# Optimization experiments

Measured on AMD Instinct MI355X. Metric: run time of the kernel, lower is better.

## Reference

```python
import jax, jax.numpy as jnp
import numpy as np

EPS = 1e-3    # Keras BatchNormalization default epsilon
ALPHA = 0.3   # Keras LeakyReLU default negative slope


def _bn(x, axes):
    # BatchNormalization(center=False, scale=False) in training mode: batch stats
    m = jnp.mean(x, axis=axes, keepdims=True)
    v = jnp.var(x, axis=axes, keepdims=True)
    return (x - m) * jax.lax.rsqrt(v + EPS)


def _leaky(x):
    return jnp.where(x > 0, x, ALPHA * x)


def setup_inputs() -> dict:
    key = jax.random.key(0)
    ks = jax.random.split(key, 8)
    B, A, D, Hid, H, hd = 8192, 16, 256, 512, 8, 64
    s = 0.02
    return {
        "state": jax.random.normal(ks[0], (B, A, D), jnp.float32),
        "agent_index": 3,
        "Ws": jax.random.normal(ks[1], (D, Hid), jnp.float32) * s,
        "bs": jnp.zeros((Hid,), jnp.float32),
        "Wc": jax.random.normal(ks[2], (D, Hid), jnp.float32) * s,
        "bc": jnp.zeros((Hid,), jnp.float32),
        "Wk": jax.random.normal(ks[3], (H, Hid, hd), jnp.float32) * s,
        "Wq": jax.random.normal(ks[4], (H, Hid, hd), jnp.float32) * s,
        "Wv": jax.random.normal(ks[5], (H, Hid, hd), jnp.float32) * s,
    }


def reference(state, agent_index, Ws, bs, Wc, bc, Wk, Wq, Wv):
    B = state.shape[0]
    H, _, hd = Wk.shape
    ai = int(agent_index)

    # current agent encoder: BN over batch, Dense, LeakyReLU -> [B, Hid]
    cur = state[:, ai, :]
    s_enc = _leaky(_bn(cur, (0,)) @ Ws + bs)

    # other agents encoder: BN over (batch, agent), Dense, LeakyReLU -> [B, A-1, Hid]
    others = jnp.concatenate([state[:, :ai, :], state[:, ai + 1:, :]], axis=1)
    sa_enc = _leaky(_bn(others, (0, 1)) @ Wc + bc)

    # batched per-head projections (replaces the python loop over heads)
    k = jnp.einsum('ban,hnd->bhad', sa_enc, Wk)           # [B,H,A-1,hd]
    v = _leaky(jnp.einsum('ban,hnd->bhad', sa_enc, Wv))   # [B,H,A-1,hd]
    q = jnp.einsum('bn,hnd->bhd', s_enc, Wq)              # [B,H,hd]

    scores = jnp.einsum('bhd,bhad->bha', q, k) / jnp.sqrt(jnp.float32(hd))
    w = jax.nn.softmax(scores, axis=-1)                   # [B,H,A-1]
    att = jnp.einsum('bha,bhad->bhd', w, v)               # [B,H,hd]

    # concat heads in order -> [B, H*hd]
    return att.reshape(B, H * hd)
```

## Files before the change

kernel.cpp:

```cpp
#include <hip/hip_runtime.h>

typedef __attribute__((ext_vector_type(8))) short short8;
typedef __attribute__((ext_vector_type(8))) unsigned short ushort8;
typedef __attribute__((ext_vector_type(4))) unsigned short bfu4;
typedef __attribute__((ext_vector_type(4))) float f32x4;

__device__ __forceinline__ unsigned short f2bf(float f){
  unsigned int u = __builtin_bit_cast(unsigned int, f);
  u += 0x7fffu + ((u >> 16) & 1u);
  return (unsigned short)(u >> 16);
}
__device__ __forceinline__ float bf2f(unsigned short h){
  unsigned int u = ((unsigned int)h) << 16;
  return __builtin_bit_cast(float, u);
}
__device__ __forceinline__ float leaky(float x){ return x > 0.f ? x : 0.3f * x; }

#define SAS 520

__global__ __launch_bounds__(1024) void ca_stats_partial(const float* __restrict__ state,
    const int* __restrict__ agp, float* __restrict__ part, int B){
  int d = threadIdx.x & 255, sl = threadIdx.x >> 8;
  int ag = agp[0];
  int bPer = (B + 255) >> 8;
  int b0 = blockIdx.x * bPer;
  float sC = 0.f, ssC = 0.f, sO = 0.f, ssO = 0.f;
  for (int b = sl; b < bPer; b += 4){
    int bb = b0 + b;
    if (bb >= B) continue;
    const float* row = state + ((size_t)bb << 12);
    #pragma unroll
    for (int a = 0; a < 16; a++){
      float v = row[a*256 + d];
      bool isC = (a == ag);
      sC  += isC ? v   : 0.f;
      ssC += isC ? v*v : 0.f;
      sO  += isC ? 0.f : v;
      ssO += isC ? 0.f : v*v;
    }
  }
  __shared__ float red[4][4][256];
  red[sl][0][d] = sC; red[sl][1][d] = ssC; red[sl][2][d] = sO; red[sl][3][d] = ssO;
  __syncthreads();
  if (sl == 0){
    float* p = part + (size_t)blockIdx.x * 1024;
    p[d]     = red[0][0][d] + red[1][0][d] + red[2][0][d] + red[3][0][d];
    p[d+256] = red[0][1][d] + red[1][1][d] + red[2][1][d] + red[3][1][d];
    p[d+512] = red[0][2][d] + red[1][2][d] + red[2][2][d] + red[3][2][d];
    p[d+768] = red[0][3][d] + red[1][3][d] + red[2][3][d] + red[3][3][d];
  }
}

__global__ __launch_bounds__(1024) void ca_stats_final(const float* __restrict__ part,
    float* __restrict__ stats, int nblk, int B){
  int d = threadIdx.x & 255, sl = threadIdx.x >> 8;
  float sC = 0.f, ssC = 0.f, sO = 0.f, ssO = 0.f;
  for (int g = sl; g < nblk; g += 4){
    const float* p = part + (size_t)g * 1024;
    sC += p[d]; ssC += p[d+256]; sO += p[d+512]; ssO += p[d+768];
  }
  __shared__ float red[4][4][256];
  red[sl][0][d] = sC; red[sl][1][d] = ssC; red[sl][2][d] = sO; red[sl][3][d] = ssO;
  __syncthreads();
  if (sl == 0){
    sC  = red[0][0][d] + red[1][0][d] + red[2][0][d] + red[3][0][d];
    ssC = red[0][1][d] + red[1][1][d] + red[2][1][d] + red[3][1][d];
    sO  = red[0][2][d] + red[1][2][d] + red[2][2][d] + red[3][2][d];
    ssO = red[0][3][d] + red[1][3][d] + red[2][3][d] + red[3][3][d];
    float nC = (float)B, nO = (float)B * 15.f;
    float mC = sC / nC, vC = ssC / nC - mC * mC;
    float mO = sO / nO, vO = ssO / nO - mO * mO;
    float rC = rsqrtf(vC + 1e-3f), rO = rsqrtf(vO + 1e-3f);
    stats[d] = rC; stats[d+256] = mC * rC; stats[d+512] = rO; stats[d+768] = mO * rO;
  }
}

__global__ __launch_bounds__(256) void ca_prep_sc(const float* __restrict__ Ws,
    const float* __restrict__ bs, const float* __restrict__ Wc, const float* __restrict__ bc,
    const float* __restrict__ stats, unsigned short* __restrict__ WsT,
    unsigned short* __restrict__ WcT, unsigned short* __restrict__ WsF,
    unsigned short* __restrict__ WcF, float* __restrict__ bsp, float* __restrict__ bcp){
  int n = blockIdx.x, d = threadIdx.x;
  float rC = stats[d], mrC = stats[d+256], rO = stats[d+512], mrO = stats[d+768];
  float ws = Ws[(size_t)d*512 + n], wc = Wc[(size_t)d*512 + n];
  unsigned short wsb = f2bf(ws * rC), wcb = f2bf(wc * rO);
  WsT[(size_t)n*256 + d] = wsb;
  WcT[(size_t)n*256 + d] = wcb;
  {
    int h = n >> 6, nt = (n >> 4) & 3, j = n & 15;
    int kk = d >> 5, hi = (d >> 3) & 3, e = d & 7;
    size_t fi = (size_t)((h*8 + kk)*4 + nt)*512 + (hi*16 + j)*8 + e;
    WsF[fi] = wsb;
    WcF[fi] = wcb;
  }
  __shared__ float red[256];
  red[d] = mrC * ws;
  __syncthreads();
  for (int s = 128; s > 0; s >>= 1){ if (d < s) red[d] += red[d+s]; __syncthreads(); }
  if (d == 0) bsp[n] = bs[n] - red[0];
  __syncthreads();
  red[d] = mrO * wc;
  __syncthreads();
  for (int s = 128; s > 0; s >>= 1){ if (d < s) red[d] += red[d+s]; __syncthreads(); }
  if (d == 0) bcp[n] = bc[n] - red[0];
}

__global__ __launch_bounds__(512) void ca_prep_kvq(const float* __restrict__ Wk,
    const float* __restrict__ Wv, const float* __restrict__ Wq,
    unsigned short* __restrict__ WkT, unsigned short* __restrict__ WvT,
    unsigned short* __restrict__ WqT, unsigned short* __restrict__ WkF2,
    unsigned short* __restrict__ WvF, unsigned short* __restrict__ WqF){
  int c = blockIdx.x & 511, m = blockIdx.x >> 9;
  int n = threadIdx.x;
  if (m == 3){
    size_t idx = (size_t)c*512 + n;
    int h = (int)(idx >> 15), nn = (int)((idx >> 6) & 511), dd = (int)(idx & 63);
    int nt = nn >> 4, j = nn & 15, kq = dd >> 5, hi = (dd >> 3) & 3, e = dd & 7;
    WkF2[(size_t)((h*32 + nt)*2 + kq)*512 + (hi*16 + j)*8 + e] = f2bf(Wk[idx]);
    return;
  }
  int h = c >> 6, dd = c & 63;
  const float* W = (m == 0) ? Wk : (m == 1) ? Wv : Wq;
  unsigned short* O = (m == 0) ? WkT : (m == 1) ? WvT : WqT;
  float scale = (m == 2) ? 0.125f : 1.f;
  unsigned short v = f2bf(W[((size_t)h*512 + n)*64 + dd] * scale);
  O[(size_t)c*512 + n] = v;
  if (m != 0){
    int nt = (c >> 4) & 3, j = c & 15;
    int kk = n >> 5, hi = (n >> 3) & 3, e = n & 7;
    size_t fi = (size_t)((h*16 + kk)*4 + nt)*512 + (hi*16 + j)*8 + e;
    if (m == 1) WvF[fi] = v; else WqF[fi] = v;
  }
}

__global__ __launch_bounds__(512) void ca_q_kernel(const float* __restrict__ state,
    const int* __restrict__ agp,
    const unsigned short* __restrict__ WsT, const float* __restrict__ bsp,
    const unsigned short* __restrict__ WqT, unsigned short* __restrict__ Qws){
  __shared__ unsigned short U[32*512];
  __shared__ float bias_s[512];
  unsigned short* Alds = U;
  unsigned short* SE = U;
  int tid = threadIdx.x, lane = tid & 63, w = tid >> 6;
  int j = lane & 15, hi = lane >> 4;
  int b0 = blockIdx.x * 32;
  int ag = agp[0];

  for (int s = tid; s < 32*32; s += 512){
    int row = s >> 5, kg = s & 31;
    const float* p = state + (((size_t)(b0 + row) * 16 + ag) << 8) + kg * 8;
    f32x4 v0 = *(const f32x4*)p, v1 = *(const f32x4*)(p + 4);
    ushort8 hv;
    hv[0]=f2bf(v0[0]); hv[1]=f2bf(v0[1]); hv[2]=f2bf(v0[2]); hv[3]=f2bf(v0[3]);
    hv[4]=f2bf(v1[0]); hv[5]=f2bf(v1[1]); hv[6]=f2bf(v1[2]); hv[7]=f2bf(v1[3]);
    *(ushort8*)&Alds[row*256 + ((kg ^ (row & 7)) << 3)] = hv;
  }
  bias_s[tid & 511] = bsp[tid & 511];
  __syncthreads();

  int cb = w * 64;
  f32x4 zero4 = {0.f, 0.f, 0.f, 0.f};
  f32x4 acc[2][4];
  #pragma unroll
  for (int a1 = 0; a1 < 2; a1++)
    #pragma unroll
    for (int a2 = 0; a2 < 4; a2++) acc[a1][a2] = zero4;

  #pragma unroll
  for (int kk = 0; kk < 8; kk++){
    short8 bfr[4];
    #pragma unroll
    for (int nt = 0; nt < 4; nt++)
      bfr[nt] = *(const short8*)&WsT[(size_t)(cb + nt*16 + j)*256 + kk*32 + hi*8];
    #pragma unroll
    for (int mt = 0; mt < 2; mt++){
      int row = mt*16 + j;
      short8 afr = *(const short8*)&Alds[row*256 + ((((kk << 2) | hi) ^ (row & 7)) << 3)];
      #pragma unroll
      for (int nt = 0; nt < 4; nt++)
        acc[mt][nt] = __builtin_amdgcn_mfma_f32_16x16x32_bf16(afr, bfr[nt], acc[mt][nt], 0, 0, 0);
    }
  }
  __syncthreads();
  #pragma unroll
  for (int mt = 0; mt < 2; mt++)
    #pragma unroll
    for (int nt = 0; nt < 4; nt++)
      #pragma unroll
      for (int i = 0; i < 4; i++){
        int row = mt*16 + hi*4 + i, col = cb + nt*16 + j;
        float x = leaky(acc[mt][nt][i] + bias_s[col]);
        SE[row*512 + ((((col >> 3) ^ (row & 7)) << 3) | (col & 7))] = f2bf(x);
      }
  __syncthreads();

  f32x4 qa[2][4];
  #pragma unroll
  for (int a1 = 0; a1 < 2; a1++)
    #pragma unroll
    for (int a2 = 0; a2 < 4; a2++) qa[a1][a2] = zero4;
  #pragma unroll
  for (int kk = 0; kk < 16; kk++){
    short8 bfr[4];
    #pragma unroll
    for (int nt = 0; nt < 4; nt++)
      bfr[nt] = *(const short8*)&WqT[(size_t)(cb + nt*16 + j)*512 + kk*32 + hi*8];
    #pragma unroll
    for (int mt = 0; mt < 2; mt++){
      int row = mt*16 + j;
      short8 afr = *(const short8*)&SE[row*512 + ((((kk << 2) | hi) ^ (row & 7)) << 3)];
      #pragma unroll
      for (int nt = 0; nt < 4; nt++)
        qa[mt][nt] = __builtin_amdgcn_mfma_f32_16x16x32_bf16(afr, bfr[nt], qa[mt][nt], 0, 0, 0);
    }
  }
  #pragma unroll
  for (int mt = 0; mt < 2; mt++)
    #pragma unroll
    for (int nt = 0; nt < 4; nt++)
      #pragma unroll
      for (int i = 0; i < 4; i++)
        Qws[(size_t)(b0 + mt*16 + hi*4 + i)*512 + cb + nt*16 + j] = f2bf(qa[mt][nt][i]);
}

__global__ __launch_bounds__(512) void ca_q_kernel_qk(const float* __restrict__ state,
    const int* __restrict__ agp,
    const unsigned short* __restrict__ WsF, const float* __restrict__ bsp,
    const unsigned short* __restrict__ WqF, const unsigned short* __restrict__ WkF2,
    unsigned short* __restrict__ QKws){
  __shared__ unsigned short U[16*SAS];
  __shared__ float bias_s[512];
  unsigned short* Alds = U;
  unsigned short* SE = U;
  unsigned short* Qlds = U;
  int tid = threadIdx.x, lane = tid & 63, w = tid >> 6;
  int j = lane & 15, hi = lane >> 4;
  int b0 = blockIdx.x * 16;
  int ag = agp[0];
  f32x4 zero4 = {0.f, 0.f, 0.f, 0.f};

  {
    int row = tid >> 5, kg = tid & 31;
    const float* p = state + (((size_t)(b0 + row) * 16 + ag) << 8) + kg * 8;
    f32x4 v0 = *(const f32x4*)p, v1 = *(const f32x4*)(p + 4);
    ushort8 hv;
    hv[0]=f2bf(v0[0]); hv[1]=f2bf(v0[1]); hv[2]=f2bf(v0[2]); hv[3]=f2bf(v0[3]);
    hv[4]=f2bf(v1[0]); hv[5]=f2bf(v1[1]); hv[6]=f2bf(v1[2]); hv[7]=f2bf(v1[3]);
    *(ushort8*)&Alds[row*256 + ((kg ^ (row & 7)) << 3)] = hv;
  }
  bias_s[tid] = bsp[tid];
  __syncthreads();

  int cb = w * 64;

  f32x4 acc[4];
  #pragma unroll
  for (int a2 = 0; a2 < 4; a2++) acc[a2] = zero4;
  #pragma unroll
  for (int kk = 0; kk < 8; kk++){
    short8 bfr[4];
    #pragma unroll
    for (int nt = 0; nt < 4; nt++)
      bfr[nt] = *(const short8*)&WsF[(size_t)((w*8 + kk)*4 + nt)*512 + lane*8];
    short8 afr = *(const short8*)&Alds[j*256 + ((((kk << 2) | hi) ^ (j & 7)) << 3)];
    #pragma unroll
    for (int nt = 0; nt < 4; nt++)
      acc[nt] = __builtin_amdgcn_mfma_f32_16x16x32_bf16(bfr[nt], afr, acc[nt], 0, 0, 0);
  }
  __syncthreads();
  #pragma unroll
  for (int nt = 0; nt < 4; nt++){
    int nb = cb + nt*16 + hi*4;
    bfu4 pk;
    #pragma unroll
    for (int i = 0; i < 4; i++) pk[i] = f2bf(leaky(acc[nt][i] + bias_s[nb + i]));
    *(bfu4*)&SE[j*SAS + nb] = pk;
  }
  __syncthreads();

  f32x4 qa[4];
  #pragma unroll
  for (int a2 = 0; a2 < 4; a2++) qa[a2] = zero4;
  #pragma unroll
  for (int kk = 0; kk < 16; kk++){
    short8 bfr[4];
    #pragma unroll
    for (int nt = 0; nt < 4; nt++)
      bfr[nt] = *(const short8*)&WqF[(size_t)((w*16 + kk)*4 + nt)*512 + lane*8];
    short8 afr = *(const short8*)&SE[j*SAS + kk*32 + hi*8];
    #pragma unroll
    for (int nt = 0; nt < 4; nt++)
      qa[nt] = __builtin_amdgcn_mfma_f32_16x16x32_bf16(bfr[nt], afr, qa[nt], 0, 0, 0);
  }
  __syncthreads();
  #pragma unroll
  for (int nt = 0; nt < 4; nt++){
    int nb = cb + nt*16 + hi*4;
    bfu4 pk;
    #pragma unroll
    for (int i = 0; i < 4; i++) pk[i] = f2bf(qa[nt][i]);
    *(bfu4*)&Qlds[j*SAS + nb] = pk;
  }
  __syncthreads();

  short8 aq[2];
  #pragma unroll
  for (int kq = 0; kq < 2; kq++)
    aq[kq] = *(const short8*)&Qlds[j*SAS + w*64 + kq*32 + hi*8];
  for (int nt = 0; nt < 32; nt++){
    short8 bf0 = *(const short8*)&WkF2[(size_t)((w*32 + nt)*2 + 0)*512 + lane*8];
    short8 bf1 = *(const short8*)&WkF2[(size_t)((w*32 + nt)*2 + 1)*512 + lane*8];
    f32x4 qt = zero4;
    qt = __builtin_amdgcn_mfma_f32_16x16x32_bf16(bf0, aq[0], qt, 0, 0, 0);
    qt = __builtin_amdgcn_mfma_f32_16x16x32_bf16(bf1, aq[1], qt, 0, 0, 0);
    bfu4 pk;
    pk[0] = f2bf(qt[0]); pk[1] = f2bf(qt[1]); pk[2] = f2bf(qt[2]); pk[3] = f2bf(qt[3]);
    *(bfu4*)&QKws[((size_t)(b0 + j)*8 + w)*512 + nt*16 + hi*4] = pk;
  }
}

__global__ __launch_bounds__(512) void ca_main_kernel_qk(const float* __restrict__ state,
    const int* __restrict__ agp,
    const unsigned short* __restrict__ WcF, const float* __restrict__ bcp,
    const unsigned short* __restrict__ WvF, const unsigned short* __restrict__ QKws,
    float* __restrict__ out){
  __shared__ unsigned short U[128*SAS];
  __shared__ float bias_s[512];
  __shared__ float Wl[8*16*8];
  unsigned short* Alds = U;
  unsigned short* SA = U;
  int tid = threadIdx.x, lane = tid & 63, w = tid >> 6;
  int j = lane & 15, hi = lane >> 4;
  int b0 = blockIdx.x * 8;
  int ag = agp[0];
  f32x4 zero4 = {0.f, 0.f, 0.f, 0.f};
  short8 zero8 = {0,0,0,0,0,0,0,0};

  #pragma unroll
  for (int g = 0; g < 2; g++){
    f32x4 st0[4], st1[4];
    #pragma unroll
    for (int it = 0; it < 4; it++){
      int s = tid + 512*(g*4 + it);
      int row = s >> 5, kg = s & 31;
      int bl = row >> 4, ai = row & 15;
      if (ai < 15){
        int a = ai + (ai >= ag ? 1 : 0);
        const float* p = state + (((size_t)(b0 + bl) * 16 + a) << 8) + kg * 8;
        st0[it] = *(const f32x4*)p;
        st1[it] = *(const f32x4*)(p + 4);
      } else { st0[it] = zero4; st1[it] = zero4; }
    }
    #pragma unroll
    for (int it = 0; it < 4; it++){
      int s = tid + 512*(g*4 + it);
      int row = s >> 5, kg = s & 31;
      ushort8 hv;
      hv[0]=f2bf(st0[it][0]); hv[1]=f2bf(st0[it][1]); hv[2]=f2bf(st0[it][2]); hv[3]=f2bf(st0[it][3]);
      hv[4]=f2bf(st1[it][0]); hv[5]=f2bf(st1[it][1]); hv[6]=f2bf(st1[it][2]); hv[7]=f2bf(st1[it][3]);
      *(ushort8*)&Alds[row*256 + ((kg ^ (row & 7)) << 3)] = hv;
    }
  }
  bias_s[tid] = bcp[tid];
  __syncthreads();

  int cb = w * 64;

  f32x4 acc[8][4];
  #pragma unroll
  for (int a1 = 0; a1 < 8; a1++)
    #pragma unroll
    for (int a2 = 0; a2 < 4; a2++) acc[a1][a2] = zero4;
  {
    short8 bcur[4], bnxt[4];
    #pragma unroll
    for (int nt = 0; nt < 4; nt++)
      bcur[nt] = *(const short8*)&WcF[(size_t)((w*8 + 0)*4 + nt)*512 + lane*8];
    #pragma unroll 1
    for (int kk = 0; kk < 8; kk++){
      if (kk < 7){
        #pragma unroll
        for (int nt = 0; nt < 4; nt++)
          bnxt[nt] = *(const short8*)&WcF[(size_t)((w*8 + kk + 1)*4 + nt)*512 + lane*8];
      }
      #pragma unroll
      for (int mt = 0; mt < 8; mt++){
        int row = mt*16 + j;
        short8 afr = *(const short8*)&Alds[row*256 + ((((kk << 2) | hi) ^ (row & 7)) << 3)];
        #pragma unroll
        for (int nt = 0; nt < 4; nt++)
          acc[mt][nt] = __builtin_amdgcn_mfma_f32_16x16x32_bf16(bcur[nt], afr, acc[mt][nt], 0, 0, 0);
      }
      #pragma unroll
      for (int nt = 0; nt < 4; nt++) bcur[nt] = bnxt[nt];
    }
  }
  __syncthreads();
  #pragma unroll
  for (int mt = 0; mt < 8; mt++)
    #pragma unroll
    for (int nt = 0; nt < 4; nt++){
      int m = mt*16 + j;
      int nb = cb + nt*16 + hi*4;
      bfu4 pk;
      #pragma unroll
      for (int i = 0; i < 4; i++) pk[i] = f2bf(leaky(acc[mt][nt][i] + bias_s[nb + i]));
      *(bfu4*)&SA[m*SAS + nb] = pk;
    }
  __syncthreads();

  f32x4 qs = zero4;
  {
    size_t qbase = ((size_t)(b0 + w)*8 + (j & 7))*512;
    #pragma unroll
    for (int kk = 0; kk < 16; kk++){
      short8 bq = *(const short8*)&QKws[qbase + kk*32 + hi*8];
      if (j >= 8) bq = zero8;
      short8 afr = *(const short8*)&SA[(w*16 + j)*SAS + kk*32 + hi*8];
      qs = __builtin_amdgcn_mfma_f32_16x16x32_bf16(afr, bq, qs, 0, 0, 0);
    }
  }
  {
    float sv0 = qs[0], sv1 = qs[1], sv2 = qs[2], sv3 = qs[3];
    sv3 = (hi == 3) ? -1e30f : sv3;
    float m = fmaxf(fmaxf(sv0, sv1), fmaxf(sv2, sv3));
    m = fmaxf(m, __shfl_xor(m, 16)); m = fmaxf(m, __shfl_xor(m, 32));
    float e0 = __expf(sv0-m), e1 = __expf(sv1-m), e2 = __expf(sv2-m), e3 = __expf(sv3-m);
    float sum = e0 + e1 + e2 + e3;
    sum += __shfl_xor(sum, 16); sum += __shfl_xor(sum, 32);
    float inv = 1.f / sum;
    if (j < 8){
      Wl[w*128 + (hi*4+0)*8 + j] = e0*inv;
      Wl[w*128 + (hi*4+1)*8 + j] = e1*inv;
      Wl[w*128 + (hi*4+2)*8 + j] = e2*inv;
      Wl[w*128 + (hi*4+3)*8 + j] = e3*inv;
    }
  }

  f32x4 va[8][4];
  #pragma unroll
  for (int a1 = 0; a1 < 8; a1++)
    #pragma unroll
    for (int a2 = 0; a2 < 4; a2++) va[a1][a2] = zero4;
  {
    short8 bcur[4], bnxt[4];
    #pragma unroll
    for (int nt = 0; nt < 4; nt++)
      bcur[nt] = *(const short8*)&WvF[(size_t)((w*16 + 0)*4 + nt)*512 + lane*8];
    #pragma unroll 1
    for (int kk = 0; kk < 16; kk++){
      if (kk < 15){
        #pragma unroll
        for (int nt = 0; nt < 4; nt++)
          bnxt[nt] = *(const short8*)&WvF[(size_t)((w*16 + kk + 1)*4 + nt)*512 + lane*8];
      }
      #pragma unroll
      for (int mt = 0; mt < 8; mt++){
        short8 afr = *(const short8*)&SA[(mt*16 + j)*SAS + kk*32 + hi*8];
        #pragma unroll
        for (int nt = 0; nt < 4; nt++)
          va[mt][nt] = __builtin_amdgcn_mfma_f32_16x16x32_bf16(afr, bcur[nt], va[mt][nt], 0, 0, 0);
      }
      #pragma unroll
      for (int nt = 0; nt < 4; nt++) bcur[nt] = bnxt[nt];
    }
  }
  __syncthreads();

  #pragma unroll
  for (int mt = 0; mt < 8; mt++){
    float w0 = Wl[mt*128 + (hi*4+0)*8 + w];
    float w1 = Wl[mt*128 + (hi*4+1)*8 + w];
    float w2 = Wl[mt*128 + (hi*4+2)*8 + w];
    float w3 = Wl[mt*128 + (hi*4+3)*8 + w];
    float ap0 = w0*leaky(va[mt][0][0]) + w1*leaky(va[mt][0][1]) + w2*leaky(va[mt][0][2]) + w3*leaky(va[mt][0][3]);
    float ap1 = w0*leaky(va[mt][1][0]) + w1*leaky(va[mt][1][1]) + w2*leaky(va[mt][1][2]) + w3*leaky(va[mt][1][3]);
    float ap2 = w0*leaky(va[mt][2][0]) + w1*leaky(va[mt][2][1]) + w2*leaky(va[mt][2][2]) + w3*leaky(va[mt][2][3]);
    float ap3 = w0*leaky(va[mt][3][0]) + w1*leaky(va[mt][3][1]) + w2*leaky(va[mt][3][2]) + w3*leaky(va[mt][3][3]);
    ap0 += __shfl_xor(ap0, 16); ap0 += __shfl_xor(ap0, 32);
    ap1 += __shfl_xor(ap1, 16); ap1 += __shfl_xor(ap1, 32);
    ap2 += __shfl_xor(ap2, 16); ap2 += __shfl_xor(ap2, 32);
    ap3 += __shfl_xor(ap3, 16); ap3 += __shfl_xor(ap3, 32);
    float val = (hi == 0) ? ap0 : (hi == 1) ? ap1 : (hi == 2) ? ap2 : ap3;
    out[(size_t)(b0 + mt)*512 + cb + lane] = val;
  }
}

__global__ __launch_bounds__(512) void ca_main_kernel(const float* __restrict__ state,
    const int* __restrict__ agp,
    const unsigned short* __restrict__ WcT, const float* __restrict__ bcp,
    const unsigned short* __restrict__ WkT, const unsigned short* __restrict__ WvT,
    const unsigned short* __restrict__ Qws, float* __restrict__ out){
  __shared__ unsigned short U[128*512];
  __shared__ unsigned short Qs[8*512];
  __shared__ float bias_s[512];
  unsigned short* Alds = U;
  unsigned short* SA = U;
  int tid = threadIdx.x, lane = tid & 63, w = tid >> 6;
  int j = lane & 15, hi = lane >> 4;
  int b0 = blockIdx.x * 8;
  int ag = agp[0];
  f32x4 zero4 = {0.f, 0.f, 0.f, 0.f};

  #pragma unroll
  for (int g = 0; g < 2; g++){
    f32x4 st0[4], st1[4];
    #pragma unroll
    for (int it = 0; it < 4; it++){
      int s = tid + 512*(g*4 + it);
      int row = s >> 5, kg = s & 31;
      int bl = row >> 4, ai = row & 15;
      if (ai < 15){
        int a = ai + (ai >= ag ? 1 : 0);
        const float* p = state + (((size_t)(b0 + bl) * 16 + a) << 8) + kg * 8;
        st0[it] = *(const f32x4*)p;
        st1[it] = *(const f32x4*)(p + 4);
      } else { st0[it] = zero4; st1[it] = zero4; }
    }
    #pragma unroll
    for (int it = 0; it < 4; it++){
      int s = tid + 512*(g*4 + it);
      int row = s >> 5, kg = s & 31;
      ushort8 hv;
      hv[0]=f2bf(st0[it][0]); hv[1]=f2bf(st0[it][1]); hv[2]=f2bf(st0[it][2]); hv[3]=f2bf(st0[it][3]);
      hv[4]=f2bf(st1[it][0]); hv[5]=f2bf(st1[it][1]); hv[6]=f2bf(st1[it][2]); hv[7]=f2bf(st1[it][3]);
      *(ushort8*)&Alds[row*256 + ((kg ^ (row & 7)) << 3)] = hv;
    }
  }
  *(ushort8*)&Qs[tid*8] = *(const ushort8*)&Qws[(size_t)b0*512 + tid*8];
  bias_s[tid] = bcp[tid];
  __syncthreads();

  int cb = w * 64;

  f32x4 acc[8][4];
  #pragma unroll
  for (int a1 = 0; a1 < 8; a1++)
    #pragma unroll
    for (int a2 = 0; a2 < 4; a2++) acc[a1][a2] = zero4;
  {
    short8 bcur[4], bnxt[4];
    #pragma unroll
    for (int nt = 0; nt < 4; nt++)
      bcur[nt] = *(const short8*)&WcT[(size_t)(cb + nt*16 + j)*256 + hi*8];
    #pragma unroll 1
    for (int kk = 0; kk < 8; kk++){
      if (kk < 7){
        #pragma unroll
        for (int nt = 0; nt < 4; nt++)
          bnxt[nt] = *(const short8*)&WcT[(size_t)(cb + nt*16 + j)*256 + (kk+1)*32 + hi*8];
      }
      #pragma unroll
      for (int mt = 0; mt < 8; mt++){
        int row = mt*16 + j;
        short8 afr = *(const short8*)&Alds[row*256 + ((((kk << 2) | hi) ^ (row & 7)) << 3)];
        #pragma unroll
        for (int nt = 0; nt < 4; nt++)
          acc[mt][nt] = __builtin_amdgcn_mfma_f32_16x16x32_bf16(afr, bcur[nt], acc[mt][nt], 0, 0, 0);
      }
      #pragma unroll
      for (int nt = 0; nt < 4; nt++) bcur[nt] = bnxt[nt];
    }
  }
  __syncthreads();
  #pragma unroll
  for (int mt = 0; mt < 8; mt++)
    #pragma unroll
    for (int nt = 0; nt < 4; nt++)
      #pragma unroll
      for (int i = 0; i < 4; i++){
        int row = mt*16 + hi*4 + i, col = cb + nt*16 + j;
        float x = leaky(acc[mt][nt][i] + bias_s[col]);
        SA[row*512 + ((((col >> 3) ^ (row & 7)) << 3) | (col & 7))] = f2bf(x);
      }
  __syncthreads();

  f32x4 ka[8][4];
  #pragma unroll
  for (int a1 = 0; a1 < 8; a1++)
    #pragma unroll
    for (int a2 = 0; a2 < 4; a2++) ka[a1][a2] = zero4;
  {
    short8 bcur[4], bnxt[4];
    #pragma unroll
    for (int nt = 0; nt < 4; nt++)
      bcur[nt] = *(const short8*)&WkT[(size_t)(cb + nt*16 + j)*512 + hi*8];
    #pragma unroll 1
    for (int kk = 0; kk < 16; kk++){
      if (kk < 15){
        #pragma unroll
        for (int nt = 0; nt < 4; nt++)
          bnxt[nt] = *(const short8*)&WkT[(size_t)(cb + nt*16 + j)*512 + (kk+1)*32 + hi*8];
      }
      #pragma unroll
      for (int mt = 0; mt < 8; mt++){
        int row = mt*16 + j;
        short8 afr = *(const short8*)&SA[row*512 + ((((kk << 2) | hi) ^ (row & 7)) << 3)];
        #pragma unroll
        for (int nt = 0; nt < 4; nt++)
          ka[mt][nt] = __builtin_amdgcn_mfma_f32_16x16x32_bf16(afr, bcur[nt], ka[mt][nt], 0, 0, 0);
      }
      #pragma unroll
      for (int nt = 0; nt < 4; nt++) bcur[nt] = bnxt[nt];
    }
  }

  float wgt[8][4];
  #pragma unroll
  for (int mt = 0; mt < 8; mt++){
    float sv[4];
    #pragma unroll
    for (int i = 0; i < 4; i++){
      float t = 0.f;
      #pragma unroll
      for (int nt = 0; nt < 4; nt++)
        t += bf2f(Qs[mt*512 + cb + nt*16 + j]) * ka[mt][nt][i];
      t += __shfl_xor(t, 1); t += __shfl_xor(t, 2);
      t += __shfl_xor(t, 4); t += __shfl_xor(t, 8);
      sv[i] = t;
    }
    sv[3] = (hi == 3) ? -1e30f : sv[3];
    float m = fmaxf(fmaxf(sv[0], sv[1]), fmaxf(sv[2], sv[3]));
    m = fmaxf(m, __shfl_xor(m, 16)); m = fmaxf(m, __shfl_xor(m, 32));
    float e0 = __expf(sv[0]-m), e1 = __expf(sv[1]-m), e2 = __expf(sv[2]-m), e3 = __expf(sv[3]-m);
    float sum = e0 + e1 + e2 + e3;
    sum += __shfl_xor(sum, 16); sum += __shfl_xor(sum, 32);
    float inv = 1.f / sum;
    wgt[mt][0] = e0*inv; wgt[mt][1] = e1*inv; wgt[mt][2] = e2*inv; wgt[mt][3] = e3*inv;
  }

  f32x4 va[8][4];
  #pragma unroll
  for (int a1 = 0; a1 < 8; a1++)
    #pragma unroll
    for (int a2 = 0; a2 < 4; a2++) va[a1][a2] = zero4;
  {
    short8 bcur[4], bnxt[4];
    #pragma unroll
    for (int nt = 0; nt < 4; nt++)
      bcur[nt] = *(const short8*)&WvT[(size_t)(cb + nt*16 + j)*512 + hi*8];
    #pragma unroll 1
    for (int kk = 0; kk < 16; kk++){
      if (kk < 15){
        #pragma unroll
        for (int nt = 0; nt < 4; nt++)
          bnxt[nt] = *(const short8*)&WvT[(size_t)(cb + nt*16 + j)*512 + (kk+1)*32 + hi*8];
      }
      #pragma unroll
      for (int mt = 0; mt < 8; mt++){
        int row = mt*16 + j;
        short8 afr = *(const short8*)&SA[row*512 + ((((kk << 2) | hi) ^ (row & 7)) << 3)];
        #pragma unroll
        for (int nt = 0; nt < 4; nt++)
          va[mt][nt] = __builtin_amdgcn_mfma_f32_16x16x32_bf16(afr, bcur[nt], va[mt][nt], 0, 0, 0);
      }
      #pragma unroll
      for (int nt = 0; nt < 4; nt++) bcur[nt] = bnxt[nt];
    }
  }

  #pragma unroll
  for (int mt = 0; mt < 8; mt++){
    float ap0 = 0.f, ap1 = 0.f, ap2 = 0.f, ap3 = 0.f;
    #pragma unroll
    for (int i = 0; i < 4; i++){
      float wv = wgt[mt][i];
      ap0 += wv * leaky(va[mt][0][i]);
      ap1 += wv * leaky(va[mt][1][i]);
      ap2 += wv * leaky(va[mt][2][i]);
      ap3 += wv * leaky(va[mt][3][i]);
    }
    ap0 += __shfl_xor(ap0, 16); ap0 += __shfl_xor(ap0, 32);
    ap1 += __shfl_xor(ap1, 16); ap1 += __shfl_xor(ap1, 32);
    ap2 += __shfl_xor(ap2, 16); ap2 += __shfl_xor(ap2, 32);
    ap3 += __shfl_xor(ap3, 16); ap3 += __shfl_xor(ap3, 32);
    float val = (hi == 0) ? ap0 : (hi == 1) ? ap1 : (hi == 2) ? ap2 : ap3;
    out[(size_t)(b0 + mt)*512 + cb + lane] = val;
  }
}

extern "C" void kernel_launch(void* const* d_in, const int* in_sizes, int n_in,
                              void* d_out, int out_size, void* d_ws, size_t ws_size,
                              hipStream_t stream) {
  const float* state = (const float*)d_in[0];
  const int*   agp   = (const int*)d_in[1];
  const float* Ws    = (const float*)d_in[2];
  const float* bs    = (const float*)d_in[3];
  const float* Wc    = (const float*)d_in[4];
  const float* bc    = (const float*)d_in[5];
  const float* Wk    = (const float*)d_in[6];
  const float* Wq    = (const float*)d_in[7];
  const float* Wv    = (const float*)d_in[8];
  float* out = (float*)d_out;
  int B = in_sizes[0] / 4096;

  char* wsb = (char*)d_ws;
  float* part  = (float*)wsb;
  float* stats = (float*)(wsb + (1 << 20));
  float* bsp   = (float*)(wsb + (1 << 20) + 4096);
  float* bcp   = (float*)(wsb + (1 << 20) + 6144);
  unsigned short* WsT  = (unsigned short*)(wsb + (1 << 20) + 8192);
  unsigned short* WcT  = WsT  + 512*256;
  unsigned short* WkT  = WcT  + 512*256;
  unsigned short* WvT  = WkT  + 512*512;
  unsigned short* WqT  = WvT  + 512*512;
  unsigned short* WkF2 = WqT  + 512*512;
  unsigned short* Qws  = WkF2 + 512*512;
  unsigned short* QKws = Qws  + (size_t)B*512;
  unsigned short* WsF  = Qws;
  unsigned short* WcF  = WsF + 512*256;
  unsigned short* WqF  = WcF + 512*256;
  unsigned short* WvF  = WqF + 512*512;

  size_t need = ((size_t)(1 << 20) + 8192)
              + 2ull*(512*256 + 512*256 + 512*512 + 512*512 + 512*512 + 512*512)
              + 2ull*B*512 + 2ull*B*8*512;
  bool qkp = (ws_size >= need);

  hipLaunchKernelGGL(ca_stats_partial, dim3(256), dim3(1024), 0, stream, state, agp, part, B);
  hipLaunchKernelGGL(ca_stats_final,   dim3(1),   dim3(1024), 0, stream, part, stats, 256, B);
  hipLaunchKernelGGL(ca_prep_sc,       dim3(512), dim3(256), 0, stream, Ws, bs, Wc, bc, stats, WsT, WcT, WsF, WcF, bsp, bcp);
  hipLaunchKernelGGL(ca_prep_kvq,      dim3(2048),dim3(512), 0, stream, Wk, Wv, Wq, WkT, WvT, WqT, WkF2, WvF, WqF);
  if (qkp){
    hipLaunchKernelGGL(ca_q_kernel_qk,   dim3(B/16),dim3(512), 0, stream, state, agp, WsF, bsp, WqF, WkF2, QKws);
    hipLaunchKernelGGL(ca_main_kernel_qk,dim3(B/8), dim3(512), 0, stream, state, agp, WcF, bcp, WvF, QKws, out);
  } else {
    hipLaunchKernelGGL(ca_q_kernel,      dim3(B/32),dim3(512), 0, stream, state, agp, WsT, bsp, WqT, Qws);
    hipLaunchKernelGGL(ca_main_kernel,   dim3(B/8), dim3(512), 0, stream, state, agp, WcT, bcp, WkT, WvT, Qws, out);
  }
}
```

Measured before the change: 234.6 us.

## Replace padded LDS rows with XOR swizzle and skip unused transposed weight writes

The shared-memory staging buffers for encoder outputs and Q in the qk kernels drop the padded row stride (520) and use a dense 512-element stride. Each 8-element chunk is XOR-swizzled by the row index, and reads and writes are updated to match. The aim is to avoid LDS bank conflicts while shrinking the shared-memory footprint. Separately, the weight-prep kernels take a flag that skips writing the transposed WsT/WcT/WkT/WvT/WqT copies when the qk path is used, which cuts redundant global stores. The added index arithmetic is small.

```diff
diff --git a/kernel.cpp b/kernel.cpp
--- a/kernel.cpp
+++ b/kernel.cpp
@@ -15,8 +15,6 @@
   return __builtin_bit_cast(float, u);
 }
 __device__ __forceinline__ float leaky(float x){ return x > 0.f ? x : 0.3f * x; }
-
-#define SAS 520
 
 __global__ __launch_bounds__(1024) void ca_stats_partial(const float* __restrict__ state,
     const int* __restrict__ agp, float* __restrict__ part, int B){
@@ -79,13 +77,16 @@
     const float* __restrict__ bs, const float* __restrict__ Wc, const float* __restrict__ bc,
     const float* __restrict__ stats, unsigned short* __restrict__ WsT,
     unsigned short* __restrict__ WcT, unsigned short* __restrict__ WsF,
-    unsigned short* __restrict__ WcF, float* __restrict__ bsp, float* __restrict__ bcp){
+    unsigned short* __restrict__ WcF, float* __restrict__ bsp, float* __restrict__ bcp,
+    int writeT){
   int n = blockIdx.x, d = threadIdx.x;
   float rC = stats[d], mrC = stats[d+256], rO = stats[d+512], mrO = stats[d+768];
   float ws = Ws[(size_t)d*512 + n], wc = Wc[(size_t)d*512 + n];
   unsigned short wsb = f2bf(ws * rC), wcb = f2bf(wc * rO);
-  WsT[(size_t)n*256 + d] = wsb;
-  WcT[(size_t)n*256 + d] = wcb;
+  if (writeT){
+    WsT[(size_t)n*256 + d] = wsb;
+    WcT[(size_t)n*256 + d] = wcb;
+  }
   {
     int h = n >> 6, nt = (n >> 4) & 3, j = n & 15;
     int kk = d >> 5, hi = (d >> 3) & 3, e = d & 7;
@@ -109,7 +110,7 @@
     const float* __restrict__ Wv, const float* __restrict__ Wq,
     unsigned short* __restrict__ WkT, unsigned short* __restrict__ WvT,
     unsigned short* __restrict__ WqT, unsigned short* __restrict__ WkF2,
-    unsigned short* __restrict__ WvF, unsigned short* __restrict__ WqF){
+    unsigned short* __restrict__ WvF, unsigned short* __restrict__ WqF, int writeT){
   int c = blockIdx.x & 511, m = blockIdx.x >> 9;
   int n = threadIdx.x;
   if (m == 3){
@@ -119,12 +120,13 @@
     WkF2[(size_t)((h*32 + nt)*2 + kq)*512 + (hi*16 + j)*8 + e] = f2bf(Wk[idx]);
     return;
   }
+  if (m == 0 && !writeT) return;
   int h = c >> 6, dd = c & 63;
   const float* W = (m == 0) ? Wk : (m == 1) ? Wv : Wq;
   unsigned short* O = (m == 0) ? WkT : (m == 1) ? WvT : WqT;
   float scale = (m == 2) ? 0.125f : 1.f;
   unsigned short v = f2bf(W[((size_t)h*512 + n)*64 + dd] * scale);
-  O[(size_t)c*512 + n] = v;
+  if (m == 0 || writeT) O[(size_t)c*512 + n] = v;
   if (m != 0){
     int nt = (c >> 4) & 3, j = c & 15;
     int kk = n >> 5, hi = (n >> 3) & 3, e = n & 7;
@@ -228,7 +230,7 @@
     const unsigned short* __restrict__ WsF, const float* __restrict__ bsp,
     const unsigned short* __restrict__ WqF, const unsigned short* __restrict__ WkF2,
     unsigned short* __restrict__ QKws){
-  __shared__ unsigned short U[16*SAS];
+  __shared__ unsigned short U[16*512];
   __shared__ float bias_s[512];
   unsigned short* Alds = U;
   unsigned short* SE = U;
@@ -271,10 +273,11 @@
   #pragma unroll
   for (int nt = 0; nt < 4; nt++){
     int nb = cb + nt*16 + hi*4;
+    int g = nb >> 3;
     bfu4 pk;
     #pragma unroll
     for (int i = 0; i < 4; i++) pk[i] = f2bf(leaky(acc[nt][i] + bias_s[nb + i]));
-    *(bfu4*)&SE[j*SAS + nb] = pk;
+    *(bfu4*)&SE[j*512 + ((g ^ (j & 7)) << 3) + (hi & 1)*4] = pk;
   }
   __syncthreads();
 
@@ -287,7 +290,7 @@
     #pragma unroll
     for (int nt = 0; nt < 4; nt++)
       bfr[nt] = *(const short8*)&WqF[(size_t)((w*16 + kk)*4 + nt)*512 + lane*8];
-    short8 afr = *(const short8*)&SE[j*SAS + kk*32 + hi*8];
+    short8 afr = *(const short8*)&SE[j*512 + ((((kk << 2) | hi) ^ (j & 7)) << 3)];
     #pragma unroll
     for (int nt = 0; nt < 4; nt++)
       qa[nt] = __builtin_amdgcn_mfma_f32_16x16x32_bf16(bfr[nt], afr, qa[nt], 0, 0, 0);
@@ -296,17 +299,20 @@
   #pragma unroll
   for (int nt = 0; nt < 4; nt++){
     int nb = cb + nt*16 + hi*4;
+    int g = nb >> 3;
     bfu4 pk;
     #pragma unroll
     for (int i = 0; i < 4; i++) pk[i] = f2bf(qa[nt][i]);
-    *(bfu4*)&Qlds[j*SAS + nb] = pk;
+    *(bfu4*)&Qlds[j*512 + ((g ^ (j & 7)) << 3) + (hi & 1)*4] = pk;
   }
   __syncthreads();
 
   short8 aq[2];
   #pragma unroll
-  for (int kq = 0; kq < 2; kq++)
-    aq[kq] = *(const short8*)&Qlds[j*SAS + w*64 + kq*32 + hi*8];
+  for (int kq = 0; kq < 2; kq++){
+    int gq = w*8 + kq*4 + hi;
+    aq[kq] = *(const short8*)&Qlds[j*512 + ((gq ^ (j & 7)) << 3)];
+  }
   for (int nt = 0; nt < 32; nt++){
     short8 bf0 = *(const short8*)&WkF2[(size_t)((w*32 + nt)*2 + 0)*512 + lane*8];
     short8 bf1 = *(const short8*)&WkF2[(size_t)((w*32 + nt)*2 + 1)*512 + lane*8];
@@ -324,7 +330,7 @@
     const unsigned short* __restrict__ WcF, const float* __restrict__ bcp,
     const unsigned short* __restrict__ WvF, const unsigned short* __restrict__ QKws,
     float* __restrict__ out){
-  __shared__ unsigned short U[128*SAS];
+  __shared__ unsigned short U[128*512];
   __shared__ float bias_s[512];
   __shared__ float Wl[8*16*8];
   unsigned short* Alds = U;
@@ -402,10 +408,11 @@
     for (int nt = 0; nt < 4; nt++){
       int m = mt*16 + j;
       int nb = cb + nt*16 + hi*4;
+      int g = nb >> 3;
       bfu4 pk;
       #pragma unroll
       for (int i = 0; i < 4; i++) pk[i] = f2bf(leaky(acc[mt][nt][i] + bias_s[nb + i]));
-      *(bfu4*)&SA[m*SAS + nb] = pk;
+      *(bfu4*)&SA[m*512 + ((g ^ (m & 7)) << 3) + (hi & 1)*4] = pk;
     }
   __syncthreads();
 
@@ -416,7 +423,8 @@
     for (int kk = 0; kk < 16; kk++){
       short8 bq = *(const short8*)&QKws[qbase + kk*32 + hi*8];
       if (j >= 8) bq = zero8;
-      short8 afr = *(const short8*)&SA[(w*16 + j)*SAS + kk*32 + hi*8];
+      int row = w*16 + j;
+      short8 afr = *(const short8*)&SA[row*512 + ((((kk << 2) | hi) ^ (row & 7)) << 3)];
       qs = __builtin_amdgcn_mfma_f32_16x16x32_bf16(afr, bq, qs, 0, 0, 0);
     }
   }
@@ -456,7 +464,8 @@
       }
       #pragma unroll
       for (int mt = 0; mt < 8; mt++){
-        short8 afr = *(const short8*)&SA[(mt*16 + j)*SAS + kk*32 + hi*8];
+        int row = mt*16 + j;
+        short8 afr = *(const short8*)&SA[row*512 + ((((kk << 2) | hi) ^ (row & 7)) << 3)];
         #pragma unroll
         for (int nt = 0; nt < 4; nt++)
           va[mt][nt] = __builtin_amdgcn_mfma_f32_16x16x32_bf16(afr, bcur[nt], va[mt][nt], 0, 0, 0);
@@ -716,11 +725,12 @@
               + 2ull*(512*256 + 512*256 + 512*512 + 512*512 + 512*512 + 512*512)
               + 2ull*B*512 + 2ull*B*8*512;
   bool qkp = (ws_size >= need);
+  int writeT = qkp ? 0 : 1;
 
   hipLaunchKernelGGL(ca_stats_partial, dim3(256), dim3(1024), 0, stream, state, agp, part, B);
   hipLaunchKernelGGL(ca_stats_final,   dim3(1),   dim3(1024), 0, stream, part, stats, 256, B);
-  hipLaunchKernelGGL(ca_prep_sc,       dim3(512), dim3(256), 0, stream, Ws, bs, Wc, bc, stats, WsT, WcT, WsF, WcF, bsp, bcp);
-  hipLaunchKernelGGL(ca_prep_kvq,      dim3(2048),dim3(512), 0, stream, Wk, Wv, Wq, WkT, WvT, WqT, WkF2, WvF, WqF);
+  hipLaunchKernelGGL(ca_prep_sc,       dim3(512), dim3(256), 0, stream, Ws, bs, Wc, bc, stats, WsT, WcT, WsF, WcF, bsp, bcp, writeT);
+  hipLaunchKernelGGL(ca_prep_kvq,      dim3(2048),dim3(512), 0, stream, Wk, Wv, Wq, WkT, WvT, WqT, WkF2, WvF, WqF, writeT);
   if (qkp){
     hipLaunchKernelGGL(ca_q_kernel_qk,   dim3(B/16),dim3(512), 0, stream, state, agp, WsF, bsp, WqF, WkF2, QKws);
     hipLaunchKernelGGL(ca_main_kernel_qk,dim3(B/8), dim3(512), 0, stream, state, agp, WcF, bcp, WvF, QKws, out);
```

New measurement: 234.2 us. About the same (-0.2%).
